# Kernel tuning notes

Measured on AMD Instinct MI355X. Metric: run time of the kernel, lower is better.

The kernel has to match this reference:

```python
import jax, jax.numpy as jnp
import numpy as np

EPS = 1e-5

def _ln(x, w, b):
    m = jnp.mean(x, axis=-1, keepdims=True)
    d = x - m
    v = jnp.mean(d * d, axis=-1, keepdims=True)
    return d * jax.lax.rsqrt(v + EPS) * w + b

def setup_inputs() -> dict:
    key = jax.random.key(0)
    ks = jax.random.split(key, 8)
    B, N, C, H = 4, 1024, 1024, 16
    D = C // H
    Hid = 4 * C
    s = 0.02
    return {
        "x": jax.random.normal(ks[0], (B, N, C), jnp.float32),
        "rel_bias": jax.random.normal(ks[1], (H, N, N), jnp.float32) * 0.02,
        "qkv_w": jax.random.normal(ks[2], (3 * C, C), jnp.float32) * s,
        "qnorm_w": jnp.ones((D,), jnp.float32), "qnorm_b": jnp.zeros((D,), jnp.float32),
        "knorm_w": jnp.ones((D,), jnp.float32), "knorm_b": jnp.zeros((D,), jnp.float32),
        "proj_w": jax.random.normal(ks[3], (C, C), jnp.float32) * s,
        "proj_b": jnp.zeros((C,), jnp.float32),
        "norm1_w": jnp.ones((C,), jnp.float32), "norm1_b": jnp.zeros((C,), jnp.float32),
        "norm2_w": jnp.ones((C,), jnp.float32), "norm2_b": jnp.zeros((C,), jnp.float32),
        "fc1_w": jax.random.normal(ks[4], (Hid, C), jnp.float32) * s,
        "fc1_b": jnp.zeros((Hid,), jnp.float32),
        "fc2_w": jax.random.normal(ks[5], (C, Hid), jnp.float32) * s,
        "fc2_b": jnp.zeros((C,), jnp.float32),
        "ls1_gamma": jnp.full((C,), 1e-5, jnp.float32),
        "ls2_gamma": jnp.full((C,), 1e-5, jnp.float32),
    }

def reference(x, rel_bias, qkv_w, qnorm_w, qnorm_b, knorm_w, knorm_b,
              proj_w, proj_b, norm1_w, norm1_b, norm2_w, norm2_b,
              fc1_w, fc1_b, fc2_w, fc2_b, ls1_gamma, ls2_gamma):
    B, N, C = x.shape
    H = rel_bias.shape[0]
    D = C // H
    scale = D ** -0.5
    # --- attention branch ---
    h = _ln(x, norm1_w, norm1_b)
    qkv = (h @ qkv_w.T).reshape(B, N, 3, H, D).transpose(2, 0, 3, 1, 4)  # [3,B,H,N,D]
    q, k, v = qkv[0], qkv[1], qkv[2]
    q = _ln(q, qnorm_w, qnorm_b)  # per-head QK LayerNorm on head_dim
    k = _ln(k, knorm_w, knorm_b)
    attn = jnp.einsum('bhnd,bhmd->bhnm', q * scale, k) + rel_bias[None]  # rel-pos bias
    attn = jax.nn.softmax(attn, axis=-1)
    o = jnp.einsum('bhnm,bhmd->bhnd', attn, v).transpose(0, 2, 1, 3).reshape(B, N, C)
    o = o @ proj_w.T + proj_b
    x = x + ls1_gamma * o  # LayerScale + residual (droppath inactive in eval)
    # --- MLP branch ---
    h2 = _ln(x, norm2_w, norm2_b)
    m = jax.nn.gelu(h2 @ fc1_w.T + fc1_b, approximate=False) @ fc2_w.T + fc2_b
    return x + ls2_gamma * m
```

## Files before the change

kernel.cpp:

```cpp
#include <hip/hip_runtime.h>
#include <hip/hip_bf16.h>


typedef __attribute__((ext_vector_type(8))) short short8;
typedef __attribute__((ext_vector_type(4))) float f32x4;

#define MFMA16(a, b, c) __builtin_amdgcn_mfma_f32_16x16x32_bf16(a, b, c, 0, 0, 0)

static __device__ __forceinline__ unsigned short f2b(float f) {
  union { __hip_bfloat16 h; unsigned short u; } cv;
  cv.h = __float2bfloat16(f);
  return cv.u;
}

static __device__ __forceinline__ void gld16(const unsigned short* g,
                                             unsigned short* l) {
  __builtin_amdgcn_global_load_lds(
      (const __attribute__((address_space(1))) void*)g,
      (__attribute__((address_space(3))) void*)l, 16, 0, 0);
}

__global__ void cvt_bf16_kernel(const float* __restrict__ in,
                                unsigned short* __restrict__ out, int n4) {
  int i = blockIdx.x * blockDim.x + threadIdx.x;
  int stride = gridDim.x * blockDim.x;
  for (; i < n4; i += stride) {
    float4 v = reinterpret_cast<const float4*>(in)[i];
    ushort4 o;
    o.x = f2b(v.x); o.y = f2b(v.y); o.z = f2b(v.z); o.w = f2b(v.w);
    reinterpret_cast<ushort4*>(out)[i] = o;
  }
}

__global__ __launch_bounds__(256) void ln_kernel(const float* __restrict__ x,
                                                 const float* __restrict__ w,
                                                 const float* __restrict__ b,
                                                 unsigned short* __restrict__ out) {
  int row = blockIdx.x, tid = threadIdx.x;
  const float* xr = x + (size_t)row * 1024;
  float4 v = reinterpret_cast<const float4*>(xr)[tid];
  float s = v.x + v.y + v.z + v.w;
  float s2 = v.x * v.x + v.y * v.y + v.z * v.z + v.w * v.w;
  for (int off = 1; off < 64; off <<= 1) {
    s += __shfl_xor(s, off);
    s2 += __shfl_xor(s2, off);
  }
  __shared__ float red[8];
  int wid = tid >> 6;
  if ((tid & 63) == 0) { red[wid] = s; red[4 + wid] = s2; }
  __syncthreads();
  s = red[0] + red[1] + red[2] + red[3];
  s2 = red[4] + red[5] + red[6] + red[7];
  float mean = s * (1.f / 1024.f);
  float rs = rsqrtf(s2 * (1.f / 1024.f) - mean * mean + 1e-5f);
  float4 wv = reinterpret_cast<const float4*>(w)[tid];
  float4 bv = reinterpret_cast<const float4*>(b)[tid];
  ushort4 o;
  o.x = f2b((v.x - mean) * rs * wv.x + bv.x);
  o.y = f2b((v.y - mean) * rs * wv.y + bv.y);
  o.z = f2b((v.z - mean) * rs * wv.z + bv.z);
  o.w = f2b((v.w - mean) * rs * wv.w + bv.w);
  reinterpret_cast<ushort4*>(out + (size_t)row * 1024)[tid] = o;
}

__global__ __launch_bounds__(256) void qkpack_kernel(
    const float* __restrict__ qkv, const float* __restrict__ qw,
    const float* __restrict__ qb, const float* __restrict__ kw,
    const float* __restrict__ kb_, unsigned short* __restrict__ Q,
    unsigned short* __restrict__ K, unsigned short* __restrict__ Vt) {
  int wid = blockIdx.x * 4 + (threadIdx.x >> 6);
  int lane = threadIdx.x & 63;
  int m = wid >> 4;
  int h = wid & 15;
  int b = m >> 10, n = m & 1023;
  const float* base = qkv + (size_t)m * 3072 + h * 64 + lane;
  float q = base[0], k = base[1024], v = base[2048];
  float qs = q, qs2 = q * q, ks = k, ks2 = k * k;
  for (int off = 1; off < 64; off <<= 1) {
    qs += __shfl_xor(qs, off); qs2 += __shfl_xor(qs2, off);
    ks += __shfl_xor(ks, off); ks2 += __shfl_xor(ks2, off);
  }
  float qm = qs * (1.f / 64.f), qv = qs2 * (1.f / 64.f) - qm * qm;
  float km = ks * (1.f / 64.f), kv = ks2 * (1.f / 64.f) - km * km;
  float qn = (q - qm) * rsqrtf(qv + 1e-5f) * qw[lane] + qb[lane];
  float kn = (k - km) * rsqrtf(kv + 1e-5f) * kw[lane] + kb_[lane];
  int bh = b * 16 + h;
  Q[((size_t)bh * 1024 + n) * 64 + lane] = f2b(qn * 0.125f);
  K[((size_t)bh * 1024 + n) * 64 + lane] = f2b(kn);
  Vt[((size_t)bh * 64 + lane) * 1024 + n] = f2b(v);
}

__global__ __launch_bounds__(256) void attn_kernel(
    const unsigned short* __restrict__ Q, const unsigned short* __restrict__ K,
    const unsigned short* __restrict__ Vt, const float* __restrict__ rb,
    unsigned short* __restrict__ O) {
  __shared__ unsigned short Ks[32][80];
  __shared__ unsigned short Vs[64][40];
  __shared__ unsigned short Ps[4][16][40];
  int bid = blockIdx.x;
  int qt = bid & 15, bh = bid >> 4;
  int h = bh & 15, b = bh >> 4;
  int q0 = qt * 64;
  int tid = threadIdx.x, lane = tid & 63, w = tid >> 6;
  int lg = lane >> 4, lr = lane & 15;

  short8 qf[2];
  {
    int qrow = q0 + w * 16 + lr;
    const unsigned short* qp = Q + ((size_t)bh * 1024 + qrow) * 64;
    qf[0] = *reinterpret_cast<const short8*>(qp + lg * 8);
    qf[1] = *reinterpret_cast<const short8*>(qp + 32 + lg * 8);
  }
  f32x4 o[4] = {};
  float mrow[4], lrow[4];
  for (int i = 0; i < 4; i++) { mrow[i] = -1e30f; lrow[i] = 0.f; }
  const float* rbh = rb + (size_t)h * 1024 * 1024;

  for (int kt = 0; kt < 32; kt++) {
    __syncthreads();
    {
      int r = tid >> 3, c = (tid & 7) * 8;
      *reinterpret_cast<short8*>(&Ks[r][c]) =
          *reinterpret_cast<const short8*>(K + ((size_t)bh * 1024 + kt * 32 + r) * 64 + c);
      int d = tid >> 2, j = (tid & 3) * 8;
      *reinterpret_cast<short8*>(&Vs[d][j]) =
          *reinterpret_cast<const short8*>(Vt + ((size_t)bh * 64 + d) * 1024 + kt * 32 + j);
    }
    __syncthreads();
    f32x4 s[2] = {};
    for (int t = 0; t < 2; t++) {
      short8 kf0 = *reinterpret_cast<const short8*>(&Ks[t * 16 + lr][lg * 8]);
      short8 kf1 = *reinterpret_cast<const short8*>(&Ks[t * 16 + lr][32 + lg * 8]);
      s[t] = MFMA16(qf[0], kf0, s[t]);
      s[t] = MFMA16(qf[1], kf1, s[t]);
    }
    int myrow = q0 + w * 16 + lg * 4;
    for (int i = 0; i < 4; i++) {
      float s0 = s[0][i] + rbh[(size_t)(myrow + i) * 1024 + kt * 32 + lr];
      float s1 = s[1][i] + rbh[(size_t)(myrow + i) * 1024 + kt * 32 + 16 + lr];
      float mx = fmaxf(s0, s1);
      for (int off = 1; off < 16; off <<= 1) mx = fmaxf(mx, __shfl_xor(mx, off));
      float mnew = fmaxf(mrow[i], mx);
      float corr = __expf(mrow[i] - mnew);
      float p0 = __expf(s0 - mnew), p1 = __expf(s1 - mnew);
      float ps = p0 + p1;
      for (int off = 1; off < 16; off <<= 1) ps += __shfl_xor(ps, off);
      lrow[i] = lrow[i] * corr + ps;
      mrow[i] = mnew;
      for (int nd = 0; nd < 4; nd++) o[nd][i] *= corr;
      Ps[w][lg * 4 + i][lr] = f2b(p0);
      Ps[w][lg * 4 + i][16 + lr] = f2b(p1);
    }
    __syncthreads();
    short8 pa = *reinterpret_cast<const short8*>(&Ps[w][lr][lg * 8]);
    for (int nd = 0; nd < 4; nd++) {
      short8 vf = *reinterpret_cast<const short8*>(&Vs[nd * 16 + lr][lg * 8]);
      o[nd] = MFMA16(pa, vf, o[nd]);
    }
  }
  for (int i = 0; i < 4; i++) {
    float inv = 1.f / lrow[i];
    int n = q0 + w * 16 + lg * 4 + i;
    size_t base = ((size_t)(b * 1024 + n)) * 1024 + h * 64;
    for (int nd = 0; nd < 4; nd++) O[base + nd * 16 + lr] = f2b(o[nd][i] * inv);
  }
}

template <int MODE>
__global__ __launch_bounds__(256) void gemm_bt(
    const unsigned short* __restrict__ A, const unsigned short* __restrict__ W,
    const float* __restrict__ bias, const float* __restrict__ resid,
    const float* __restrict__ gamma, float* __restrict__ outF,
    unsigned short* __restrict__ outB, int M, int Nn, int Kd) {
  __shared__ unsigned short As[128 * 32];
  __shared__ unsigned short Bs[128 * 32];
  int tid = threadIdx.x;
  int lane = tid & 63, wv = tid >> 6;
  int wm = wv >> 1, wn = wv & 1;
  int lg = lane >> 4, lr = lane & 15;
  int m0 = blockIdx.y * 128, n0 = blockIdx.x * 128;
  f32x4 acc[4][4] = {};
  int lrow = lane >> 2;
  int lcol = (lane & 3) * 8;
  int c0 = wv * 16, c1 = 64 + wv * 16;
  const unsigned short* Ab = A + (size_t)(m0 + lrow) * Kd + lcol;
  const unsigned short* Wb = W + (size_t)(n0 + lrow) * Kd + lcol;
  for (int k0 = 0; k0 < Kd; k0 += 32) {
    __syncthreads();
    gld16(Ab + (size_t)c0 * Kd + k0, &As[c0 * 32]);
    gld16(Ab + (size_t)c1 * Kd + k0, &As[c1 * 32]);
    gld16(Wb + (size_t)c0 * Kd + k0, &Bs[c0 * 32]);
    gld16(Wb + (size_t)c1 * Kd + k0, &Bs[c1 * 32]);
    __syncthreads();
    short8 af[4], bf[4];
    for (int i = 0; i < 4; i++)
      af[i] = *reinterpret_cast<const short8*>(&As[(wm * 64 + i * 16 + lr) * 32 + lg * 8]);
    for (int i = 0; i < 4; i++)
      bf[i] = *reinterpret_cast<const short8*>(&Bs[(wn * 64 + i * 16 + lr) * 32 + lg * 8]);
    for (int mi = 0; mi < 4; mi++)
      for (int ni = 0; ni < 4; ni++)
        acc[mi][ni] = MFMA16(af[mi], bf[ni], acc[mi][ni]);
  }
  int row0 = m0 + wm * 64, col0 = n0 + wn * 64;
  for (int mi = 0; mi < 4; mi++)
    for (int ni = 0; ni < 4; ni++) {
      int col = col0 + ni * 16 + lr;
      int rbase = row0 + mi * 16 + lg * 4;
      for (int i = 0; i < 4; i++) {
        int row = rbase + i;
        float v = acc[mi][ni][i];
        if (MODE == 0) {
          outF[(size_t)row * Nn + col] = v;
        } else if (MODE == 1) {
          outF[(size_t)row * Nn + col] =
              resid[(size_t)row * Nn + col] + gamma[col] * (v + bias[col]);
        } else {
          float t = v + bias[col];
          float g = 0.5f * t * (1.f + erff(t * 0.70710678f));
          outB[(size_t)row * Nn + col] = f2b(g);
        }
      }
    }
}

extern "C" void kernel_launch(void* const* d_in, const int* in_sizes, int n_in,
                              void* d_out, int out_size, void* d_ws, size_t ws_size,
                              hipStream_t stream) {
  const float* x      = (const float*)d_in[0];
  const float* relb   = (const float*)d_in[1];
  const float* qkv_w  = (const float*)d_in[2];
  const float* qnw    = (const float*)d_in[3];
  const float* qnb    = (const float*)d_in[4];
  const float* knw    = (const float*)d_in[5];
  const float* knb    = (const float*)d_in[6];
  const float* proj_w = (const float*)d_in[7];
  const float* proj_b = (const float*)d_in[8];
  const float* n1w    = (const float*)d_in[9];
  const float* n1b    = (const float*)d_in[10];
  const float* n2w    = (const float*)d_in[11];
  const float* n2b    = (const float*)d_in[12];
  const float* fc1_w  = (const float*)d_in[13];
  const float* fc1_b  = (const float*)d_in[14];
  const float* fc2_w  = (const float*)d_in[15];
  const float* fc2_b  = (const float*)d_in[16];
  const float* ls1    = (const float*)d_in[17];
  const float* ls2    = (const float*)d_in[18];
  float* out = (float*)d_out;

  char* ws = (char*)d_ws;
  size_t off = 0;
  auto take = [&](size_t bytes) {
    char* p = ws + off;
    off += (bytes + 255) & ~(size_t)255;
    return p;
  };
  unsigned short* h     = (unsigned short*)take((size_t)4096 * 1024 * 2);
  unsigned short* wqkv  = (unsigned short*)take((size_t)3072 * 1024 * 2);
  unsigned short* wproj = (unsigned short*)take((size_t)1024 * 1024 * 2);
  unsigned short* wfc1  = (unsigned short*)take((size_t)4096 * 1024 * 2);
  unsigned short* wfc2  = (unsigned short*)take((size_t)4096 * 1024 * 2);
  float*          qkvb  = (float*)take((size_t)4096 * 3072 * 4);
  unsigned short* Q     = (unsigned short*)take((size_t)64 * 1024 * 64 * 2);
  unsigned short* Kb    = (unsigned short*)take((size_t)64 * 1024 * 64 * 2);
  unsigned short* Vt    = (unsigned short*)take((size_t)64 * 64 * 1024 * 2);
  unsigned short* ao    = (unsigned short*)take((size_t)4096 * 1024 * 2);
  float*          x1    = (float*)take((size_t)4096 * 1024 * 4);
  unsigned short* h2 = h;
  unsigned short* m1 = (unsigned short*)qkvb;

  cvt_bf16_kernel<<<1024, 256, 0, stream>>>(qkv_w, wqkv, 3072 * 1024 / 4);
  cvt_bf16_kernel<<<1024, 256, 0, stream>>>(proj_w, wproj, 1024 * 1024 / 4);
  cvt_bf16_kernel<<<1024, 256, 0, stream>>>(fc1_w, wfc1, 4096 * 1024 / 4);
  cvt_bf16_kernel<<<1024, 256, 0, stream>>>(fc2_w, wfc2, 4096 * 1024 / 4);

  ln_kernel<<<4096, 256, 0, stream>>>(x, n1w, n1b, h);
  gemm_bt<0><<<dim3(24, 32), 256, 0, stream>>>(h, wqkv, nullptr, nullptr, nullptr,
                                               qkvb, nullptr, 4096, 3072, 1024);
  qkpack_kernel<<<16384, 256, 0, stream>>>(qkvb, qnw, qnb, knw, knb, Q, Kb, Vt);
  attn_kernel<<<1024, 256, 0, stream>>>(Q, Kb, Vt, relb, ao);
  gemm_bt<1><<<dim3(8, 32), 256, 0, stream>>>(ao, wproj, proj_b, x, ls1, x1,
                                              nullptr, 4096, 1024, 1024);
  ln_kernel<<<4096, 256, 0, stream>>>(x1, n2w, n2b, h2);
  gemm_bt<2><<<dim3(32, 32), 256, 0, stream>>>(h2, wfc1, fc1_b, nullptr, nullptr,
                                               nullptr, m1, 4096, 4096, 1024);
  gemm_bt<1><<<dim3(8, 32), 256, 0, stream>>>(m1, wfc2, fc2_b, x1, ls2, out,
                                              nullptr, 4096, 1024, 4096);
}
```

Measured before the change: 515.9 us.

## Double-buffer GEMM LDS staging, swizzle block order, use BM=64 tiles for narrow GEMMs

Restructures the bf16 GEMM so the next K-slice is prefetched into a second LDS buffer via global_load_lds while MFMAs run on the current one, with one waitcnt+barrier per iteration. It also remaps the 1D block index with an XCD-style swizzle for cache locality, and uses a 64-row tile for the N=1024 GEMMs so those launches have twice as many blocks. The aim is to hide global-load latency and improve occupancy and L2 reuse, at the cost of doubled LDS and more index math.

```diff
diff --git a/kernel.cpp b/kernel.cpp
--- a/kernel.cpp
+++ b/kernel.cpp
@@ -18,6 +18,12 @@
   __builtin_amdgcn_global_load_lds(
       (const __attribute__((address_space(1))) void*)g,
       (__attribute__((address_space(3))) void*)l, 16, 0, 0);
+}
+
+static __device__ __forceinline__ void drain_dma_then_barrier() {
+  asm volatile("s_waitcnt vmcnt(0)" ::: "memory");
+  __builtin_amdgcn_sched_barrier(0);
+  __syncthreads();
 }
 
 __global__ void cvt_bf16_kernel(const float* __restrict__ in,
@@ -166,43 +172,73 @@
   }
 }
 
-template <int MODE>
+template <int MODE, int BM>
 __global__ __launch_bounds__(256) void gemm_bt(
     const unsigned short* __restrict__ A, const unsigned short* __restrict__ W,
     const float* __restrict__ bias, const float* __restrict__ resid,
     const float* __restrict__ gamma, float* __restrict__ outF,
     unsigned short* __restrict__ outB, int M, int Nn, int Kd) {
-  __shared__ unsigned short As[128 * 32];
-  __shared__ unsigned short Bs[128 * 32];
+  constexpr int BN = 128;
+  constexpr int MI = BM / 32;
+  constexpr int ACH = BM / 16;
+  constexpr int TCH = ACH + BN / 16;
+  constexpr int CPW = TCH / 4;
+  __shared__ unsigned short S[2][(BM + BN) * 32];
   int tid = threadIdx.x;
   int lane = tid & 63, wv = tid >> 6;
   int wm = wv >> 1, wn = wv & 1;
   int lg = lane >> 4, lr = lane & 15;
-  int m0 = blockIdx.y * 128, n0 = blockIdx.x * 128;
-  f32x4 acc[4][4] = {};
+  int nbx = Nn >> 7;
+  int cpx = gridDim.x >> 3;
+  int swz = (blockIdx.x & 7) * cpx + (blockIdx.x >> 3);
+  int m0 = (swz / nbx) * BM, n0 = (swz % nbx) * BN;
+  f32x4 acc[MI][4] = {};
   int lrow = lane >> 2;
   int lcol = (lane & 3) * 8;
-  int c0 = wv * 16, c1 = 64 + wv * 16;
-  const unsigned short* Ab = A + (size_t)(m0 + lrow) * Kd + lcol;
-  const unsigned short* Wb = W + (size_t)(n0 + lrow) * Kd + lcol;
+  const unsigned short* gbase[CPW];
+#pragma unroll
+  for (int i = 0; i < CPW; i++) {
+    int c = wv + i * 4;
+    gbase[i] = (c < ACH)
+        ? A + (size_t)(m0 + c * 16 + lrow) * Kd + lcol
+        : W + (size_t)(n0 + (c - ACH) * 16 + lrow) * Kd + lcol;
+  }
+  auto stage = [&](int buf, int k0) {
+#pragma unroll
+    for (int i = 0; i < CPW; i++) {
+      int c = wv + i * 4;
+      gld16(gbase[i] + k0, &S[buf][c * 512]);
+    }
+  };
+  stage(0, 0);
+  drain_dma_then_barrier();
+  int cur = 0;
   for (int k0 = 0; k0 < Kd; k0 += 32) {
-    __syncthreads();
-    gld16(Ab + (size_t)c0 * Kd + k0, &As[c0 * 32]);
-    gld16(Ab + (size_t)c1 * Kd + k0, &As[c1 * 32]);
-    gld16(Wb + (size_t)c0 * Kd + k0, &Bs[c0 * 32]);
-    gld16(Wb + (size_t)c1 * Kd + k0, &Bs[c1 * 32]);
-    __syncthreads();
-    short8 af[4], bf[4];
+    int nxt = cur ^ 1;
+    if (k0 + 32 < Kd) stage(nxt, k0 + 32);
+    const unsigned short* Sa = &S[cur][0];
+    const unsigned short* Sb = &S[cur][BM * 32];
+    short8 af[MI], bf[4];
+#pragma unroll
+    for (int i = 0; i < MI; i++)
+      af[i] = *reinterpret_cast<const short8*>(
+          &Sa[(wm * (BM / 2) + i * 16 + lr) * 32 + lg * 8]);
+#pragma unroll
     for (int i = 0; i < 4; i++)
-      af[i] = *reinterpret_cast<const short8*>(&As[(wm * 64 + i * 16 + lr) * 32 + lg * 8]);
-    for (int i = 0; i < 4; i++)
-      bf[i] = *reinterpret_cast<const short8*>(&Bs[(wn * 64 + i * 16 + lr) * 32 + lg * 8]);
-    for (int mi = 0; mi < 4; mi++)
+      bf[i] = *reinterpret_cast<const short8*>(
+          &Sb[(wn * 64 + i * 16 + lr) * 32 + lg * 8]);
+#pragma unroll
+    for (int mi = 0; mi < MI; mi++)
+#pragma unroll
       for (int ni = 0; ni < 4; ni++)
         acc[mi][ni] = MFMA16(af[mi], bf[ni], acc[mi][ni]);
-  }
-  int row0 = m0 + wm * 64, col0 = n0 + wn * 64;
-  for (int mi = 0; mi < 4; mi++)
+    drain_dma_then_barrier();
+    cur = nxt;
+  }
+  int row0 = m0 + wm * (BM / 2), col0 = n0 + wn * 64;
+#pragma unroll
+  for (int mi = 0; mi < MI; mi++)
+#pragma unroll
     for (int ni = 0; ni < 4; ni++) {
       int col = col0 + ni * 16 + lr;
       int rbase = row0 + mi * 16 + lg * 4;
@@ -274,15 +310,15 @@
   cvt_bf16_kernel<<<1024, 256, 0, stream>>>(fc2_w, wfc2, 4096 * 1024 / 4);
 
   ln_kernel<<<4096, 256, 0, stream>>>(x, n1w, n1b, h);
-  gemm_bt<0><<<dim3(24, 32), 256, 0, stream>>>(h, wqkv, nullptr, nullptr, nullptr,
-                                               qkvb, nullptr, 4096, 3072, 1024);
+  gemm_bt<0, 128><<<768, 256, 0, stream>>>(h, wqkv, nullptr, nullptr, nullptr,
+                                           qkvb, nullptr, 4096, 3072, 1024);
   qkpack_kernel<<<16384, 256, 0, stream>>>(qkvb, qnw, qnb, knw, knb, Q, Kb, Vt);
   attn_kernel<<<1024, 256, 0, stream>>>(Q, Kb, Vt, relb, ao);
-  gemm_bt<1><<<dim3(8, 32), 256, 0, stream>>>(ao, wproj, proj_b, x, ls1, x1,
-                                              nullptr, 4096, 1024, 1024);
+  gemm_bt<1, 64><<<512, 256, 0, stream>>>(ao, wproj, proj_b, x, ls1, x1,
+                                          nullptr, 4096, 1024, 1024);
   ln_kernel<<<4096, 256, 0, stream>>>(x1, n2w, n2b, h2);
-  gemm_bt<2><<<dim3(32, 32), 256, 0, stream>>>(h2, wfc1, fc1_b, nullptr, nullptr,
-                                               nullptr, m1, 4096, 4096, 1024);
-  gemm_bt<1><<<dim3(8, 32), 256, 0, stream>>>(m1, wfc2, fc2_b, x1, ls2, out,
-                                              nullptr, 4096, 1024, 4096);
-}
+  gemm_bt<2, 128><<<1024, 256, 0, stream>>>(h2, wfc1, fc1_b, nullptr, nullptr,
+                                            nullptr, m1, 4096, 4096, 1024);
+  gemm_bt<1, 64><<<512, 256, 0, stream>>>(m1, wfc2, fc2_b, x1, ls2, out,
+                                          nullptr, 4096, 1024, 4096);
+}
```

After: 475.8 us. 7.8% less time.
